# Optimization experiments

Hardware: AMD Instinct MI355X
Metric: run time of the kernel (lower is better)

## Reference

```python
import jax, jax.numpy as jnp
import numpy as np

N, L = 4, 512
DN = 128   # node_feat_dim
DP = 64    # pair_feat_dim
H = 8      # num_heads
HD = 32    # hidden_dim per head
EPS = 1e-5


def _layer_norm(x, g, b):
    m = jnp.mean(x, axis=-1, keepdims=True)
    v = jnp.var(x, axis=-1, keepdims=True)
    return (x - m) / jnp.sqrt(v + EPS) * g + b


def setup_inputs() -> dict:
    key = jax.random.key(0)
    ks = jax.random.split(key, 12)
    w = lambda k, shape: (jax.random.normal(k, shape, jnp.float32)
                          / np.float32(np.sqrt(shape[0])))
    return {
        "x": jax.random.normal(ks[0], (N, L, DN), jnp.float32),
        "z": jax.random.normal(ks[1], (N, L, L, DP), jnp.float32),
        "Wq": w(ks[2], (DN, H * HD)),
        "Wk": w(ks[3], (DN, H * HD)),
        "Wv": w(ks[4], (DN, H * HD)),
        "Wp": w(ks[5], (DP, H)),
        "Wt1": w(ks[6], (H * HD + H * DP, DN)),
        "bt1": jnp.zeros((DN,), jnp.float32),
        "g1": jnp.ones((DN,), jnp.float32),
        "b1": jnp.zeros((DN,), jnp.float32),
        "W2a": w(ks[7], (DN, DN)),
        "b2a": jnp.zeros((DN,), jnp.float32),
        "W2b": w(ks[8], (DN, DN)),
        "b2b": jnp.zeros((DN,), jnp.float32),
        "g2": jnp.ones((DN,), jnp.float32),
        "b2": jnp.zeros((DN,), jnp.float32),
    }


def reference(x, z, Wq, Wk, Wv, Wp, Wt1, bt1, g1, b1,
              W2a, b2a, W2b, b2b, g2, b2):
    # projections -> (N, L, H, HD)
    q = (x @ Wq).reshape(N, L, H, HD)
    k = (x @ Wk).reshape(N, L, H, HD)
    v = (x @ Wv).reshape(N, L, H, HD)
    # pairwise node logits: (N, Li, Lj, H)
    logits_node = jnp.einsum('nihd,njhd->nijh', q, k) / np.float32(np.sqrt(HD))
    logits_pair = z @ Wp                                    # (N, Li, Lj, H)
    logits = (logits_node + logits_pair) * np.float32(np.sqrt(0.5))
    alpha = jax.nn.softmax(logits, axis=2)                  # softmax over j
    # aggregation
    feat_node = jnp.einsum('nijh,njhd->nihd', alpha, v).reshape(N, L, H * HD)
    feat_pair = jnp.einsum('nijh,nijp->nihp', alpha, z).reshape(N, L, H * DP)
    agg = jnp.concatenate([feat_node, feat_pair], axis=-1)  # (N, L, H*HD + H*DP)
    feats = _layer_norm(x + agg @ Wt1 + bt1, g1, b1)
    out = jax.nn.relu(feats @ W2a + b2a) @ W2b + b2b
    return _layer_norm(feats + out, g2, b2)
```

## Files before the change

### kernel.cpp

```cpp
#include <hip/hip_runtime.h>
#include <math.h>

#define NB 4
#define L 512
#define DN 128
#define DP 64
#define H 8
#define HD 32
#define NH (H*HD)
#define AGG (NH + H*DP)
#define JC 64
#define NCH (L/JC)

__device__ float g_qT[(size_t)NB*H*L*HD];
__device__ float g_kT[(size_t)NB*H*L*HD];
__device__ float g_v[NB*L*NH];
__device__ float g_agg[NB*L*AGG];
__device__ float g_nl[(size_t)NB*H*L*L];

__global__ __launch_bounds__(256) void k_qkv(const float* __restrict__ x,
    const float* __restrict__ Wq, const float* __restrict__ Wk,
    const float* __restrict__ Wv)
{
    __shared__ float xs[4*DN];
    int t = threadIdx.x;
    int rowbase = blockIdx.x * 4;
    #pragma unroll
    for (int it = 0; it < 2; ++it) {
        int flat = it*256 + t;
        xs[flat] = x[(size_t)rowbase*DN + flat];
    }
    __syncthreads();
    float aq[4], ak[4], av[4];
    #pragma unroll
    for (int r = 0; r < 4; ++r) { aq[r]=0.f; ak[r]=0.f; av[r]=0.f; }
    for (int d = 0; d < DN; ++d) {
        float wq = Wq[d*NH + t];
        float wk = Wk[d*NH + t];
        float wv = Wv[d*NH + t];
        #pragma unroll
        for (int r = 0; r < 4; ++r) {
            float xv = xs[r*DN + d];
            aq[r] = fmaf(xv, wq, aq[r]);
            ak[r] = fmaf(xv, wk, ak[r]);
            av[r] = fmaf(xv, wv, av[r]);
        }
    }
    int n2 = rowbase >> 9;
    int i0 = rowbase & 511;
    int h = t >> 5, d = t & 31;
    #pragma unroll
    for (int r = 0; r < 4; ++r) {
        size_t base = ((size_t)(n2*H + h)*L + i0 + r)*HD + d;
        g_qT[base] = aq[r] * 0.125f;
        g_kT[base] = ak[r];
        g_v[(size_t)(rowbase+r)*NH + t] = av[r];
    }
}

__global__ __launch_bounds__(256) void k_qk()
{
    __shared__ __align__(16) float qs[16*36];
    int t = threadIdx.x;
    int bid = blockIdx.x;
    int n = bid >> 8;
    int h = (bid >> 5) & 7;
    int i0 = (bid & 31) << 4;
    const float* qTb = g_qT + (size_t)((n*H + h)*L + i0)*HD;
    if (t < 128) {
        int row = t >> 3, c4 = (t & 7) << 2;
        float4 qv = *(const float4*)(qTb + row*HD + c4);
        *(float4*)&qs[row*36 + c4] = qv;
    }
    __syncthreads();
    const float* kTb = g_kT + (size_t)(n*H + h)*L*HD;
    for (int jc = 0; jc < L; jc += 256) {
        int j = jc + t;
        float4 kr[8];
        const float4* kb = (const float4*)(kTb + (size_t)j*HD);
        #pragma unroll
        for (int c4 = 0; c4 < 8; ++c4) kr[c4] = kb[c4];
        float* outb = g_nl + (size_t)((n*H + h)*L + i0)*L + j;
        #pragma unroll 4
        for (int i = 0; i < 16; ++i) {
            float a0 = 0.f, a1 = 0.f;
            #pragma unroll
            for (int c4 = 0; c4 < 8; c4 += 2) {
                float4 q0 = *(const float4*)&qs[i*36 + c4*4];
                float4 q1 = *(const float4*)&qs[i*36 + c4*4 + 4];
                a0 = fmaf(q0.x, kr[c4].x,   fmaf(q0.y, kr[c4].y,   a0));
                a0 = fmaf(q0.z, kr[c4].z,   fmaf(q0.w, kr[c4].w,   a0));
                a1 = fmaf(q1.x, kr[c4+1].x, fmaf(q1.y, kr[c4+1].y, a1));
                a1 = fmaf(q1.z, kr[c4+1].z, fmaf(q1.w, kr[c4+1].w, a1));
            }
            outb[(size_t)i*L] = a0 + a1;
        }
    }
}

#define ATTN_STEP(c, cur, NC0, NC4, NN0, NN4)                                  \
  {                                                                            \
    __syncthreads();                                                           \
    if ((c)+1 < NCH) {                                                         \
      _Pragma("unroll")                                                        \
      for (int it2 = 0; it2 < 4; ++it2) {                                      \
        int f4 = it2*256 + t, jj = f4 >> 4, p4 = (f4 & 15) << 2;               \
        float* d = &zc[(cur)^1][jj*65 + p4];                                   \
        d[0]=zR[it2].x; d[1]=zR[it2].y; d[2]=zR[it2].z; d[3]=zR[it2].w;        \
      }                                                                        \
    }                                                                          \
    if ((c)+2 < NCH) {                                                         \
      const float4* s2 = (const float4*)(zrow + (size_t)((c)+2)*JC*DP);        \
      zR[0]=s2[t]; zR[1]=s2[256+t]; zR[2]=s2[512+t]; zR[3]=s2[768+t];          \
    }                                                                          \
    if ((c)+1 < NCH) {                                                         \
      int jg2 = ((c)+1)*JC + lane;                                             \
      NN0 = nl0[jg2]; NN4 = nl4[jg2];                                          \
    }                                                                          \
    float va = NC0, vb = NC4;                                                  \
    {                                                                          \
      const float* zr = &zc[cur][lane*65];                                     \
      _Pragma("unroll 16")                                                     \
      for (int pp = 0; pp < DP; ++pp) {                                        \
        float zv = zr[pp];                                                     \
        va = fmaf(zv, wp[pp*H + wv],     va);                                  \
        vb = fmaf(zv, wp[pp*H + wv + 4], vb);                                  \
      }                                                                        \
    }                                                                          \
    float ma = va, mb = vb;                                                    \
    _Pragma("unroll")                                                          \
    for (int o = 32; o > 0; o >>= 1) {                                         \
      ma = fmaxf(ma, __shfl_xor(ma, o));                                       \
      mb = fmaxf(mb, __shfl_xor(mb, o));                                       \
    }                                                                          \
    float mna = fmaxf(m0, ma), mnb = fmaxf(m1, mb);                            \
    float ra = __expf(m0 - mna), rb = __expf(m1 - mnb);                        \
    float ea = __expf(va - mna), eb = __expf(vb - mnb);                        \
    lcw[wv][0][lane] = ea; lcw[wv][1][lane] = eb;                              \
    float sa = ea, sb = eb;                                                    \
    _Pragma("unroll")                                                          \
    for (int o = 32; o > 0; o >>= 1) {                                         \
      sa += __shfl_xor(sa, o); sb += __shfl_xor(sb, o);                        \
    }                                                                          \
    s0 = s0*ra + sa; s1 = s1*rb + sb; m0 = mna; m1 = mnb;                      \
    float rsel = hiHalf ? rb : ra;                                             \
    accN *= rsel; accP0 *= ra; accP1 *= rb;                                    \
    const float* vbase = g_v + (size_t)(n*L + (c)*JC)*NH + hoff;               \
    const float* zcc = zc[cur];                                                \
    _Pragma("unroll 8")                                                        \
    for (int j = 0; j < JC; ++j) {                                             \
      float la = lcw[wv][0][j];                                                \
      float lb = lcw[wv][1][j];                                                \
      float vv = vbase[(size_t)j*NH];                                          \
      float zv = zcc[j*65 + lane];                                             \
      float lsel = hiHalf ? lb : la;                                           \
      accN  = fmaf(lsel, vv, accN);                                            \
      accP0 = fmaf(la, zv, accP0);                                             \
      accP1 = fmaf(lb, zv, accP1);                                             \
    }                                                                          \
  }

__global__ __launch_bounds__(256) void k_attn(const float* __restrict__ z,
    const float* __restrict__ Wp)
{
    __shared__ float zc[2][JC*65];
    __shared__ float lcw[4][2][JC];
    __shared__ float wp[DP*H];

    int t = threadIdx.x;
    int lane = t & 63;
    int wv = t >> 6;
    int row = blockIdx.x;
    int n = row >> 9;
    int i = row & 511;
    const float* zrow = z + (size_t)row * (L*DP);

    wp[t]       = Wp[t]       * 0.70710678118654752f;
    wp[t + 256] = Wp[t + 256] * 0.70710678118654752f;

    const float* nl0 = g_nl + (size_t)((n*H + wv    )*L + i)*L;
    const float* nl4 = g_nl + (size_t)((n*H + wv + 4)*L + i)*L;

    bool hiHalf = (lane >= 32);
    int hoff = wv*32 + lane + (hiHalf ? 96 : 0);

    float accN = 0.f, accP0 = 0.f, accP1 = 0.f;
    float m0 = -1e30f, s0 = 0.f, m1 = -1e30f, s1 = 0.f;

    float4 zR[4];
    float nlc0, nlc4, nln0, nln4;

    {
        float4 zP[4];
        const float4* sp0 = (const float4*)zrow;
        #pragma unroll
        for (int it = 0; it < 4; ++it) zP[it] = sp0[it*256 + t];
        nlc0 = nl0[lane]; nlc4 = nl4[lane];
        #pragma unroll
        for (int it = 0; it < 4; ++it) {
            int f4 = it*256 + t, jj = f4 >> 4, p4 = (f4 & 15) << 2;
            float* d = &zc[0][jj*65 + p4];
            d[0]=zP[it].x; d[1]=zP[it].y; d[2]=zP[it].z; d[3]=zP[it].w;
        }
        const float4* sp1 = (const float4*)(zrow + (size_t)JC*DP);
        #pragma unroll
        for (int it = 0; it < 4; ++it) zR[it] = sp1[it*256 + t];
    }
    ATTN_STEP(0,0,nlc0,nlc4,nln0,nln4)
    ATTN_STEP(1,1,nln0,nln4,nlc0,nlc4)
    ATTN_STEP(2,0,nlc0,nlc4,nln0,nln4)
    ATTN_STEP(3,1,nln0,nln4,nlc0,nlc4)
    ATTN_STEP(4,0,nlc0,nlc4,nln0,nln4)
    ATTN_STEP(5,1,nln0,nln4,nlc0,nlc4)
    ATTN_STEP(6,0,nlc0,nlc4,nln0,nln4)
    ATTN_STEP(7,1,nln0,nln4,nlc0,nlc4)

    float* arow = g_agg + (size_t)row * AGG;
    float sn = hiHalf ? s1 : s0;
    arow[hoff]                  = accN  * (1.f / sn);
    arow[NH + wv*DP + lane]     = accP0 * (1.f / s0);
    arow[NH + (wv+4)*DP + lane] = accP1 * (1.f / s1);
}

__global__ __launch_bounds__(256) void k_mlp(const float* __restrict__ x,
    const float* __restrict__ Wt1, const float* __restrict__ bt1,
    const float* __restrict__ g1, const float* __restrict__ b1,
    const float* __restrict__ W2a, const float* __restrict__ b2a,
    const float* __restrict__ W2b, const float* __restrict__ b2b,
    const float* __restrict__ g2, const float* __restrict__ b2,
    float* __restrict__ out)
{
    __shared__ float aggL[4*AGG];
    __shared__ float featsL[4*132];
    __shared__ float h1L[4*132];
    int t = threadIdx.x;
    int tc = t & 127;
    int tr = t >> 7;
    int lane = t & 63, wv = t >> 6;
    int rowbase = blockIdx.x * 4;

    #pragma unroll
    for (int it = 0; it < 12; ++it) {
        int flat = it*256 + t;
        aggL[flat] = g_agg[(size_t)rowbase*AGG + flat];
    }
    __syncthreads();
    float acc[2] = {0.f,0.f};
    for (int kk = 0; kk < AGG; ++kk) {
        float w = Wt1[kk*DN + tc];
        #pragma unroll
        for (int r = 0; r < 2; ++r)
            acc[r] = fmaf(aggL[(tr*2+r)*AGG + kk], w, acc[r]);
    }
    float bt = bt1[tc];
    #pragma unroll
    for (int r = 0; r < 2; ++r) {
        int row = tr*2 + r;
        featsL[row*132 + tc] = acc[r] + bt + x[(size_t)(rowbase+row)*DN + tc];
    }
    __syncthreads();
    {
        int row = wv;
        float v0 = featsL[row*132 + lane];
        float v1 = featsL[row*132 + 64 + lane];
        float s = v0 + v1, s2 = v0*v0 + v1*v1;
        #pragma unroll
        for (int o = 32; o > 0; o >>= 1) {
            s  += __shfl_xor(s,  o);
            s2 += __shfl_xor(s2, o);
        }
        float mean = s * (1.f/128.f);
        float var  = s2 * (1.f/128.f) - mean*mean;
        float rstd = rsqrtf(var + 1e-5f);
        featsL[row*132 + lane]      = (v0 - mean)*rstd*g1[lane]      + b1[lane];
        featsL[row*132 + 64 + lane] = (v1 - mean)*rstd*g1[64+lane]   + b1[64+lane];
    }
    __syncthreads();
    float acc2[2] = {0.f,0.f};
    for (int kk = 0; kk < DN; ++kk) {
        float w = W2a[kk*DN + tc];
        #pragma unroll
        for (int r = 0; r < 2; ++r)
            acc2[r] = fmaf(featsL[(tr*2+r)*132 + kk], w, acc2[r]);
    }
    float ba = b2a[tc];
    #pragma unroll
    for (int r = 0; r < 2; ++r)
        h1L[(tr*2+r)*132 + tc] = fmaxf(acc2[r] + ba, 0.f);
    __syncthreads();
    float acc3[2] = {0.f,0.f};
    for (int kk = 0; kk < DN; ++kk) {
        float w = W2b[kk*DN + tc];
        #pragma unroll
        for (int r = 0; r < 2; ++r)
            acc3[r] = fmaf(h1L[(tr*2+r)*132 + kk], w, acc3[r]);
    }
    float bb = b2b[tc];
    #pragma unroll
    for (int r = 0; r < 2; ++r) {
        int row = tr*2 + r;
        featsL[row*132 + tc] = featsL[row*132 + tc] + acc3[r] + bb;
    }
    __syncthreads();
    {
        int row = wv;
        float v0 = featsL[row*132 + lane];
        float v1 = featsL[row*132 + 64 + lane];
        float s = v0 + v1, s2 = v0*v0 + v1*v1;
        #pragma unroll
        for (int o = 32; o > 0; o >>= 1) {
            s  += __shfl_xor(s,  o);
            s2 += __shfl_xor(s2, o);
        }
        float mean = s * (1.f/128.f);
        float var  = s2 * (1.f/128.f) - mean*mean;
        float rstd = rsqrtf(var + 1e-5f);
        out[(size_t)(rowbase+row)*DN + lane]      = (v0 - mean)*rstd*g2[lane]    + b2[lane];
        out[(size_t)(rowbase+row)*DN + 64 + lane] = (v1 - mean)*rstd*g2[64+lane] + b2[64+lane];
    }
}

extern "C" void kernel_launch(void* const* d_in, const int* in_sizes, int n_in,
                              void* d_out, int out_size, void* d_ws, size_t ws_size,
                              hipStream_t stream) {
    const float* x   = (const float*)d_in[0];
    const float* z   = (const float*)d_in[1];
    const float* Wq  = (const float*)d_in[2];
    const float* Wk  = (const float*)d_in[3];
    const float* Wv  = (const float*)d_in[4];
    const float* Wp  = (const float*)d_in[5];
    const float* Wt1 = (const float*)d_in[6];
    const float* bt1 = (const float*)d_in[7];
    const float* g1  = (const float*)d_in[8];
    const float* b1  = (const float*)d_in[9];
    const float* W2a = (const float*)d_in[10];
    const float* b2a = (const float*)d_in[11];
    const float* W2b = (const float*)d_in[12];
    const float* b2b = (const float*)d_in[13];
    const float* g2  = (const float*)d_in[14];
    const float* b2  = (const float*)d_in[15];
    float* out = (float*)d_out;

    k_qkv<<<NB*L/4, 256, 0, stream>>>(x, Wq, Wk, Wv);
    k_qk<<<NB*H*(L/16), 256, 0, stream>>>();
    k_attn<<<NB*L, 256, 0, stream>>>(z, Wp);
    k_mlp<<<NB*L/4, 256, 0, stream>>>(x, Wt1, bt1, g1, b1,
                                      W2a, b2a, W2b, b2b, g2, b2, out);
}
```

Measured before the change: 196.5 us.

## Halve attention chunk size and split heads across wave halves for logits

The attention j-chunk shrinks from 64 to 32 so each wave-half of 32 lanes now computes logits and online softmax for one head, instead of every lane computing two heads. This removes redundant per-lane work in the pair-logit dot product and the shuffle reductions, and it lowers z staging registers and LDS footprint. In exchange there are twice as many chunk steps, and so twice as many barriers and rescale operations, and the per-half softmax factors must be broadcast with extra shuffles.

```diff
diff --git a/kernel.cpp b/kernel.cpp
--- a/kernel.cpp
+++ b/kernel.cpp
@@ -9,7 +9,7 @@
 #define HD 32
 #define NH (H*HD)
 #define AGG (NH + H*DP)
-#define JC 64
+#define JC 32
 #define NCH (L/JC)
 
 __device__ float g_qT[(size_t)NB*H*L*HD];
@@ -98,12 +98,12 @@
     }
 }
 
-#define ATTN_STEP(c, cur, NC0, NC4, NN0, NN4)                                  \
+#define ATTN_STEP(c, cur, NC, NN)                                              \
   {                                                                            \
     __syncthreads();                                                           \
     if ((c)+1 < NCH) {                                                         \
       _Pragma("unroll")                                                        \
-      for (int it2 = 0; it2 < 4; ++it2) {                                      \
+      for (int it2 = 0; it2 < 2; ++it2) {                                      \
         int f4 = it2*256 + t, jj = f4 >> 4, p4 = (f4 & 15) << 2;               \
         float* d = &zc[(cur)^1][jj*65 + p4];                                   \
         d[0]=zR[it2].x; d[1]=zR[it2].y; d[2]=zR[it2].z; d[3]=zR[it2].w;        \
@@ -111,40 +111,34 @@
     }                                                                          \
     if ((c)+2 < NCH) {                                                         \
       const float4* s2 = (const float4*)(zrow + (size_t)((c)+2)*JC*DP);        \
-      zR[0]=s2[t]; zR[1]=s2[256+t]; zR[2]=s2[512+t]; zR[3]=s2[768+t];          \
+      zR[0]=s2[t]; zR[1]=s2[256+t];                                            \
     }                                                                          \
-    if ((c)+1 < NCH) {                                                         \
-      int jg2 = ((c)+1)*JC + lane;                                             \
-      NN0 = nl0[jg2]; NN4 = nl4[jg2];                                          \
-    }                                                                          \
-    float va = NC0, vb = NC4;                                                  \
+    if ((c)+1 < NCH) { NN = nlh[((c)+1)*JC + l32]; }                           \
+    float va = NC, va1 = 0.f;                                                  \
     {                                                                          \
-      const float* zr = &zc[cur][lane*65];                                     \
+      const float* zr = &zc[cur][l32*65];                                      \
       _Pragma("unroll 16")                                                     \
-      for (int pp = 0; pp < DP; ++pp) {                                        \
-        float zv = zr[pp];                                                     \
-        va = fmaf(zv, wp[pp*H + wv],     va);                                  \
-        vb = fmaf(zv, wp[pp*H + wv + 4], vb);                                  \
+      for (int pp = 0; pp < DP; pp += 2) {                                     \
+        va  = fmaf(zr[pp],   wp[pp*H     + myh], va);                          \
+        va1 = fmaf(zr[pp+1], wp[(pp+1)*H + myh], va1);                         \
       }                                                                        \
     }                                                                          \
-    float ma = va, mb = vb;                                                    \
+    va += va1;                                                                 \
+    float mx = va;                                                             \
     _Pragma("unroll")                                                          \
-    for (int o = 32; o > 0; o >>= 1) {                                         \
-      ma = fmaxf(ma, __shfl_xor(ma, o));                                       \
-      mb = fmaxf(mb, __shfl_xor(mb, o));                                       \
-    }                                                                          \
-    float mna = fmaxf(m0, ma), mnb = fmaxf(m1, mb);                            \
-    float ra = __expf(m0 - mna), rb = __expf(m1 - mnb);                        \
-    float ea = __expf(va - mna), eb = __expf(vb - mnb);                        \
-    lcw[wv][0][lane] = ea; lcw[wv][1][lane] = eb;                              \
-    float sa = ea, sb = eb;                                                    \
+    for (int o = 16; o > 0; o >>= 1)                                           \
+      mx = fmaxf(mx, __shfl_xor(mx, o));                                       \
+    float mn = fmaxf(mh, mx);                                                  \
+    float r  = __expf(mh - mn);                                                \
+    float e  = __expf(va - mn);                                                \
+    lcw[wv][hiHalf][l32] = e;                                                  \
+    float se = e;                                                              \
     _Pragma("unroll")                                                          \
-    for (int o = 32; o > 0; o >>= 1) {                                         \
-      sa += __shfl_xor(sa, o); sb += __shfl_xor(sb, o);                        \
-    }                                                                          \
-    s0 = s0*ra + sa; s1 = s1*rb + sb; m0 = mna; m1 = mnb;                      \
-    float rsel = hiHalf ? rb : ra;                                             \
-    accN *= rsel; accP0 *= ra; accP1 *= rb;                                    \
+    for (int o = 16; o > 0; o >>= 1)                                           \
+      se += __shfl_xor(se, o);                                                 \
+    sh = sh*r + se; mh = mn;                                                   \
+    float ra = __shfl(r, 0), rb = __shfl(r, 32);                               \
+    accN *= r; accP0 *= ra; accP1 *= rb;                                       \
     const float* vbase = g_v + (size_t)(n*L + (c)*JC)*NH + hoff;               \
     const float* zcc = zc[cur];                                                \
     _Pragma("unroll 8")                                                        \
@@ -153,8 +147,7 @@
       float lb = lcw[wv][1][j];                                                \
       float vv = vbase[(size_t)j*NH];                                          \
       float zv = zcc[j*65 + lane];                                             \
-      float lsel = hiHalf ? lb : la;                                           \
-      accN  = fmaf(lsel, vv, accN);                                            \
+      accN  = fmaf(hiHalf ? lb : la, vv, accN);                                \
       accP0 = fmaf(la, zv, accP0);                                             \
       accP1 = fmaf(lb, zv, accP1);                                             \
     }                                                                          \
@@ -178,46 +171,53 @@
     wp[t]       = Wp[t]       * 0.70710678118654752f;
     wp[t + 256] = Wp[t + 256] * 0.70710678118654752f;
 
-    const float* nl0 = g_nl + (size_t)((n*H + wv    )*L + i)*L;
-    const float* nl4 = g_nl + (size_t)((n*H + wv + 4)*L + i)*L;
-
-    bool hiHalf = (lane >= 32);
+    int hiHalf = lane >> 5;
+    int l32 = lane & 31;
+    int myh = wv + 4*hiHalf;
+    const float* nlh = g_nl + ((size_t)((n*H + myh)*L + i))*L;
+
     int hoff = wv*32 + lane + (hiHalf ? 96 : 0);
 
     float accN = 0.f, accP0 = 0.f, accP1 = 0.f;
-    float m0 = -1e30f, s0 = 0.f, m1 = -1e30f, s1 = 0.f;
-
-    float4 zR[4];
-    float nlc0, nlc4, nln0, nln4;
+    float mh = -1e30f, sh = 0.f;
+
+    float4 zR[2];
+    float nlc, nln;
 
     {
-        float4 zP[4];
+        float4 zP[2];
         const float4* sp0 = (const float4*)zrow;
-        #pragma unroll
-        for (int it = 0; it < 4; ++it) zP[it] = sp0[it*256 + t];
-        nlc0 = nl0[lane]; nlc4 = nl4[lane];
-        #pragma unroll
-        for (int it = 0; it < 4; ++it) {
+        zP[0] = sp0[t]; zP[1] = sp0[256 + t];
+        nlc = nlh[l32];
+        #pragma unroll
+        for (int it = 0; it < 2; ++it) {
             int f4 = it*256 + t, jj = f4 >> 4, p4 = (f4 & 15) << 2;
             float* d = &zc[0][jj*65 + p4];
             d[0]=zP[it].x; d[1]=zP[it].y; d[2]=zP[it].z; d[3]=zP[it].w;
         }
         const float4* sp1 = (const float4*)(zrow + (size_t)JC*DP);
-        #pragma unroll
-        for (int it = 0; it < 4; ++it) zR[it] = sp1[it*256 + t];
-    }
-    ATTN_STEP(0,0,nlc0,nlc4,nln0,nln4)
-    ATTN_STEP(1,1,nln0,nln4,nlc0,nlc4)
-    ATTN_STEP(2,0,nlc0,nlc4,nln0,nln4)
-    ATTN_STEP(3,1,nln0,nln4,nlc0,nlc4)
-    ATTN_STEP(4,0,nlc0,nlc4,nln0,nln4)
-    ATTN_STEP(5,1,nln0,nln4,nlc0,nlc4)
-    ATTN_STEP(6,0,nlc0,nlc4,nln0,nln4)
-    ATTN_STEP(7,1,nln0,nln4,nlc0,nlc4)
-
+        zR[0] = sp1[t]; zR[1] = sp1[256 + t];
+    }
+    ATTN_STEP(0 ,0,nlc,nln)
+    ATTN_STEP(1 ,1,nln,nlc)
+    ATTN_STEP(2 ,0,nlc,nln)
+    ATTN_STEP(3 ,1,nln,nlc)
+    ATTN_STEP(4 ,0,nlc,nln)
+    ATTN_STEP(5 ,1,nln,nlc)
+    ATTN_STEP(6 ,0,nlc,nln)
+    ATTN_STEP(7 ,1,nln,nlc)
+    ATTN_STEP(8 ,0,nlc,nln)
+    ATTN_STEP(9 ,1,nln,nlc)
+    ATTN_STEP(10,0,nlc,nln)
+    ATTN_STEP(11,1,nln,nlc)
+    ATTN_STEP(12,0,nlc,nln)
+    ATTN_STEP(13,1,nln,nlc)
+    ATTN_STEP(14,0,nlc,nln)
+    ATTN_STEP(15,1,nln,nlc)
+
+    float s0 = __shfl(sh, 0), s1 = __shfl(sh, 32);
     float* arow = g_agg + (size_t)row * AGG;
-    float sn = hiHalf ? s1 : s0;
-    arow[hoff]                  = accN  * (1.f / sn);
+    arow[hoff]                  = accN  * (1.f / sh);
     arow[NH + wv*DP + lane]     = accP0 * (1.f / s0);
     arow[NH + (wv+4)*DP + lane] = accP1 * (1.f / s1);
 }
```

Measured after the change: 205.1 us. 1.04x slower.
